# Kernel tuning notes

Measured on AMD Instinct MI355X. Metric: run time of the kernel, lower is better.

Reference implementation:

```python
import jax, jax.numpy as jnp
import numpy as np

NH, NKV, HD, RANK = 16, 4, 128, 512
DIM = NH * HD
EPS = 1.1920928955078125e-07  # torch float32 eps used by F.rms_norm default


def _rms_norm(x):
    return x * jax.lax.rsqrt(jnp.mean(x * x, axis=-1, keepdims=True) + EPS)


def _rope(x, cos, sin):
    # x: [B,H,T,HD]; cos/sin: [T,HD//2]
    h = x.shape[-1] // 2
    x1, x2 = x[..., :h], x[..., h:]
    return jnp.concatenate((x1 * cos + x2 * sin, -x1 * sin + x2 * cos), axis=-1)


def setup_inputs() -> dict:
    key = jax.random.key(0)
    ks = jax.random.split(key, 7)
    B, T = 2, 2048
    s = DIM ** -0.5
    x = jax.random.normal(ks[0], (B, T, DIM), dtype=jnp.float32)
    Wq = jax.random.normal(ks[1], (DIM, DIM), dtype=jnp.float32) * s
    Wdown = jax.random.normal(ks[2], (RANK, DIM), dtype=jnp.float32) * s
    Wkup = jax.random.normal(ks[3], (NKV * HD, RANK), dtype=jnp.float32) * s
    Wvup = jax.random.normal(ks[4], (NKV * HD, RANK), dtype=jnp.float32) * s
    Wproj = jax.random.normal(ks[5], (DIM, DIM), dtype=jnp.float32) * s
    q_gain = jnp.full((NH,), 1.0, dtype=jnp.float32)
    return {"x": x, "Wq": Wq, "Wdown": Wdown, "Wkup": Wkup, "Wvup": Wvup,
            "Wproj": Wproj, "q_gain": q_gain}


def reference(x, Wq, Wdown, Wkup, Wvup, Wproj, q_gain):
    B, T, _ = x.shape
    # q projection -> [B,NH,T,HD], rms-norm per head dim
    q = (x @ Wq.T).reshape(B, T, NH, HD).transpose(0, 2, 1, 3)
    q = _rms_norm(q)
    # low-rank latent kv
    lat = x @ Wdown.T                                   # [B,T,RANK]
    k = (lat @ Wkup.T).reshape(B, T, NKV, HD).transpose(0, 2, 1, 3)
    v = (lat @ Wvup.T).reshape(B, T, NKV, HD).transpose(0, 2, 1, 3)
    k = _rms_norm(k)
    # rotary embeddings
    inv_freq = 1.0 / (10000.0 ** (jnp.arange(0, HD, 2, dtype=jnp.float32) / HD))
    t = jnp.arange(T, dtype=jnp.float32)
    f = jnp.outer(t, inv_freq)                          # [T,HD//2]
    cos, sin = jnp.cos(f), jnp.sin(f)
    q, k = _rope(q, cos, sin), _rope(k, cos, sin)
    q = q * q_gain[None, :, None, None]
    # GQA repeat_interleave kv heads
    rep = NH // NKV
    k = jnp.repeat(k, rep, axis=1)
    v = jnp.repeat(v, rep, axis=1)
    # causal SDPA
    scores = jnp.einsum('bhqd,bhkd->bhqk', q, k) / np.sqrt(HD).astype(np.float32)
    causal = jnp.tril(jnp.ones((T, T), dtype=bool))
    scores = jnp.where(causal, scores, jnp.finfo(scores.dtype).min)
    attn = jax.nn.softmax(scores, axis=-1)
    y = jnp.einsum('bhqk,bhkd->bhqd', attn, v)          # [B,NH,T,HD]
    y = y.transpose(0, 2, 1, 3).reshape(B, T, NH * HD)
    return y @ Wproj.T
```

## Files before the change

### kernel.cpp

```cpp
#include <hip/hip_runtime.h>
#include <stdint.h>

#define B_    2
#define T_    2048
#define NH_   16
#define NKV_  4
#define HD_   128
#define RANK_ 512
#define DIM_  2048
#define BT_   (B_*T_)
#define EPS_  1.1920928955078125e-07f
#define LOG2E_ 1.4426950408889634f
#define CT_   6
#define SLOTS_PER_BH_ 204

typedef __bf16 bf16x8 __attribute__((ext_vector_type(8)));
typedef float  f32x4  __attribute__((ext_vector_type(4)));

__device__ inline unsigned short f2bf(float f) {
    unsigned int u = __float_as_uint(f);
    u += 0x7fff + ((u >> 16) & 1);
    return (unsigned short)(u >> 16);
}
__device__ inline float bf2f(unsigned short u) {
    return __uint_as_float(((unsigned int)u) << 16);
}
__device__ inline float fast_exp2(float x) { return __builtin_amdgcn_exp2f(x); }

#define GLOAD_LDS16(gp, lp)                                                        \
    __builtin_amdgcn_global_load_lds(                                              \
        (const __attribute__((address_space(1))) void*)(gp),                       \
        (__attribute__((address_space(3))) void*)(lp), 16, 0, 0)

struct CvtArgs {
    const float* src[6];
    unsigned short* dst[6];
    int start4[6];
};
__global__ __launch_bounds__(256) void cvt_all(CvtArgs a, int total4) {
    int i = blockIdx.x * 256 + threadIdx.x;
    if (i >= total4) return;
    int s = 0;
#pragma unroll
    for (int k = 1; k < 6; k++) s += (i >= a.start4[k]) ? 1 : 0;
    int j = i - a.start4[s];
    float4 v = ((const float4*)a.src[s])[j];
    ushort4 o;
    o.x = f2bf(v.x); o.y = f2bf(v.y); o.z = f2bf(v.z); o.w = f2bf(v.w);
    ((ushort4*)a.dst[s])[j] = o;
}

__device__ inline void store_out(float* p, float v) { *p = v; }
__device__ inline void store_out(unsigned short* p, float v) { *p = f2bf(v); }

template <typename OT>
__global__ __launch_bounds__(256) void gemm_bt(const unsigned short* __restrict__ A,
                                               const unsigned short* __restrict__ W,
                                               OT* __restrict__ C,
                                               int M, int N, int K) {
    __shared__ unsigned short As[2][128][32];
    __shared__ unsigned short Ws[2][128][32];
    int tid  = threadIdx.x;
    int lane = tid & 63, wave = tid >> 6;
    int quad = lane >> 4, l16 = lane & 15;
    int wm = (wave >> 1) * 64, wn = (wave & 1) * 64;
    long m0 = (long)blockIdx.y * 128, n0 = (long)blockIdx.x * 128;

    int sr = wave * 32 + (lane >> 2);
    int scl = (lane & 3) * 8;
    const unsigned short* Ag0 = A + (m0 + sr) * K + scl;
    const unsigned short* Ag1 = A + (m0 + sr + 16) * K + scl;
    const unsigned short* Wg0 = W + (n0 + sr) * K + scl;
    const unsigned short* Wg1 = W + (n0 + sr + 16) * K + scl;
    unsigned short* Al0 = &As[0][wave * 32][0];
    unsigned short* Al1 = &As[0][wave * 32 + 16][0];
    unsigned short* Wl0 = &Ws[0][wave * 32][0];
    unsigned short* Wl1 = &Ws[0][wave * 32 + 16][0];

    f32x4 acc[4][4];
#pragma unroll
    for (int i = 0; i < 4; i++)
#pragma unroll
        for (int j = 0; j < 4; j++) acc[i][j] = (f32x4){0.f, 0.f, 0.f, 0.f};

    for (int k0 = 0; k0 < K; k0 += 64) {
        __syncthreads();
        GLOAD_LDS16(Ag0 + k0, Al0);
        GLOAD_LDS16(Ag1 + k0, Al1);
        GLOAD_LDS16(Wg0 + k0, Wl0);
        GLOAD_LDS16(Wg1 + k0, Wl1);
        GLOAD_LDS16(Ag0 + k0 + 32, Al0 + 4096);
        GLOAD_LDS16(Ag1 + k0 + 32, Al1 + 4096);
        GLOAD_LDS16(Wg0 + k0 + 32, Wl0 + 4096);
        GLOAD_LDS16(Wg1 + k0 + 32, Wl1 + 4096);
        __syncthreads();
#pragma unroll
        for (int p = 0; p < 2; p++) {
            bf16x8 af[4], wf[4];
#pragma unroll
            for (int i = 0; i < 4; i++) af[i] = *(const bf16x8*)&As[p][wm + i * 16 + l16][quad * 8];
#pragma unroll
            for (int j = 0; j < 4; j++) wf[j] = *(const bf16x8*)&Ws[p][wn + j * 16 + l16][quad * 8];
#pragma unroll
            for (int i = 0; i < 4; i++)
#pragma unroll
                for (int j = 0; j < 4; j++)
                    acc[i][j] = __builtin_amdgcn_mfma_f32_16x16x32_bf16(af[i], wf[j], acc[i][j], 0, 0, 0);
        }
    }
#pragma unroll
    for (int i = 0; i < 4; i++)
#pragma unroll
        for (int j = 0; j < 4; j++)
#pragma unroll
            for (int r = 0; r < 4; r++) {
                long row = m0 + wm + i * 16 + quad * 4 + r;
                long col = n0 + wn + j * 16 + l16;
                store_out(&C[row * N + col], acc[i][j][r]);
            }
}

__global__ __launch_bounds__(256) void gemm_split(const unsigned short* __restrict__ A,
                                                  const unsigned short* __restrict__ W,
                                                  unsigned short* __restrict__ C1, int N1,
                                                  unsigned short* __restrict__ C2,
                                                  int M, int N, int K) {
    __shared__ unsigned short As[2][128][32];
    __shared__ unsigned short Ws[2][128][32];
    int tid  = threadIdx.x;
    int lane = tid & 63, wave = tid >> 6;
    int quad = lane >> 4, l16 = lane & 15;
    int wm = (wave >> 1) * 64, wn = (wave & 1) * 64;
    long m0 = (long)blockIdx.y * 128, n0 = (long)blockIdx.x * 128;

    int sr = wave * 32 + (lane >> 2);
    int scl = (lane & 3) * 8;
    const unsigned short* Ag0 = A + (m0 + sr) * K + scl;
    const unsigned short* Ag1 = A + (m0 + sr + 16) * K + scl;
    const unsigned short* Wg0 = W + (n0 + sr) * K + scl;
    const unsigned short* Wg1 = W + (n0 + sr + 16) * K + scl;
    unsigned short* Al0 = &As[0][wave * 32][0];
    unsigned short* Al1 = &As[0][wave * 32 + 16][0];
    unsigned short* Wl0 = &Ws[0][wave * 32][0];
    unsigned short* Wl1 = &Ws[0][wave * 32 + 16][0];

    f32x4 acc[4][4];
#pragma unroll
    for (int i = 0; i < 4; i++)
#pragma unroll
        for (int j = 0; j < 4; j++) acc[i][j] = (f32x4){0.f, 0.f, 0.f, 0.f};

    for (int k0 = 0; k0 < K; k0 += 64) {
        __syncthreads();
        GLOAD_LDS16(Ag0 + k0, Al0);
        GLOAD_LDS16(Ag1 + k0, Al1);
        GLOAD_LDS16(Wg0 + k0, Wl0);
        GLOAD_LDS16(Wg1 + k0, Wl1);
        GLOAD_LDS16(Ag0 + k0 + 32, Al0 + 4096);
        GLOAD_LDS16(Ag1 + k0 + 32, Al1 + 4096);
        GLOAD_LDS16(Wg0 + k0 + 32, Wl0 + 4096);
        GLOAD_LDS16(Wg1 + k0 + 32, Wl1 + 4096);
        __syncthreads();
#pragma unroll
        for (int p = 0; p < 2; p++) {
            bf16x8 af[4], wf[4];
#pragma unroll
            for (int i = 0; i < 4; i++) af[i] = *(const bf16x8*)&As[p][wm + i * 16 + l16][quad * 8];
#pragma unroll
            for (int j = 0; j < 4; j++) wf[j] = *(const bf16x8*)&Ws[p][wn + j * 16 + l16][quad * 8];
#pragma unroll
            for (int i = 0; i < 4; i++)
#pragma unroll
                for (int j = 0; j < 4; j++)
                    acc[i][j] = __builtin_amdgcn_mfma_f32_16x16x32_bf16(af[i], wf[j], acc[i][j], 0, 0, 0);
        }
    }
    unsigned short* Cb;
    long ldc, nb;
    if (n0 < N1) { Cb = C1; ldc = N1;     nb = n0; }
    else         { Cb = C2; ldc = N - N1; nb = n0 - N1; }
#pragma unroll
    for (int i = 0; i < 4; i++)
#pragma unroll
        for (int j = 0; j < 4; j++)
#pragma unroll
            for (int r = 0; r < 4; r++) {
                long row = m0 + wm + i * 16 + quad * 4 + r;
                long col = nb + wn + j * 16 + l16;
                Cb[row * ldc + col] = f2bf(acc[i][j][r]);
            }
}

__global__ __launch_bounds__(256) void prep_all(const unsigned short* __restrict__ q_lin,
                                                const unsigned short* __restrict__ kv_lin,
                                                const float* __restrict__ gain,
                                                unsigned short* __restrict__ q_bf,
                                                unsigned short* __restrict__ k_bf,
                                                unsigned short* __restrict__ vt) {
    int bid = blockIdx.x;
    if (bid < 20480) {
        bool isQ = bid < 16384;
        int nheads = isQ ? NH_ : NKV_;
        int incols = isQ ? DIM_ : 1024;
        const unsigned short* lin = isQ ? q_lin : kv_lin;
        unsigned short* out = isQ ? q_bf : k_bf;
        int base = isQ ? bid : bid - 16384;
        int r    = base * 4 + (threadIdx.x >> 6);
        int lane = threadIdx.x & 63;
        int bt = r / nheads, h = r % nheads;
        const unsigned short* ip = lin + (long)bt * incols + h * 128;
        float x1 = bf2f(ip[lane]), x2 = bf2f(ip[lane + 64]);
        float ss = x1 * x1 + x2 * x2;
#pragma unroll
        for (int off = 32; off; off >>= 1) ss += __shfl_xor(ss, off);
        float inv = rsqrtf(ss * (1.0f / 128.0f) + EPS_);
        x1 *= inv; x2 *= inv;
        int b = bt / T_, t = bt % T_;
        float freq = expf(-(float)lane * 0.14391156463f);
        float f = (float)t * freq;
        float s, c;
        sincosf(f, &s, &c);
        float g = isQ ? gain[h] * 0.08838834764831845f * LOG2E_ : 1.0f;
        float o1 = (x1 * c + x2 * s) * g;
        float o2 = (x2 * c - x1 * s) * g;
        unsigned short* op = out + ((long)(b * nheads + h) * T_ + t) * 128;
        op[lane]      = f2bf(o1);
        op[lane + 64] = f2bf(o2);
    } else {
        __shared__ unsigned short tile[32][33];
        int idx = bid - 20480;
        int tt = idx & 63, dd = (idx >> 6) & 3, bkv = idx >> 8;
        int b = bkv >> 2, kv = bkv & 3;
        int t0 = tt * 32, d0 = dd * 32;
        int tx = threadIdx.x & 31, ty = threadIdx.x >> 5;
#pragma unroll
        for (int rr = 0; rr < 32; rr += 8) {
            int t = t0 + ty + rr;
            tile[ty + rr][tx] = kv_lin[((long)(b * T_ + t)) * 1024 + 512 + kv * 128 + d0 + tx];
        }
        __syncthreads();
#pragma unroll
        for (int rr = 0; rr < 32; rr += 8) {
            int d = d0 + ty + rr;
            vt[((long)((b * NKV_ + kv) * 128 + d)) * T_ + t0 + tx] = tile[tx][ty + rr];
        }
    }
}

__global__ __launch_bounds__(256, 3) void attn_kernel(const unsigned short* __restrict__ Q,
                                                      const unsigned short* __restrict__ Km,
                                                      const unsigned short* __restrict__ Vt,
                                                      unsigned short* __restrict__ po,
                                                      float* __restrict__ pm,
                                                      float* __restrict__ pl) {
    __shared__ alignas(16) unsigned short Vs2[2][128][32];
    __shared__ alignas(16) unsigned short KsPt[4 * 32 * 72];

    int tid = threadIdx.x, lane = tid & 63, wave = tid >> 6;
    int quad = lane >> 4, l16 = lane & 15;

    int g8 = blockIdx.x & 7;
    int j5 = blockIdx.x >> 3;
    int hh = j5 / 51;
    int rem = 50 - (j5 % 51);
    int b = g8 >> 2, kvh = g8 & 3, h = kvh * 4 + hh, bh = b * 16 + h;
    int a = 0;
    while (a < 5 && 3 * (a + 1) * (a + 2) / 2 <= rem) a++;
    int off = rem - 3 * a * (a + 1) / 2;
    int nc = a + 1;
    int qb = (a == 5) ? 15 : (3 * a + off / nc);
    int c  = (a == 5) ? off : (off % nc);
    int Q0 = qb * 128 + wave * 32;

    int kt0 = c * CT_;
    int nt  = min(CT_, 2 * qb + 2 - kt0);

    const unsigned short* qp = Q + ((long)(b * NH_ + h) * T_ + Q0) * 128;
    const char* kb = (const char*)(Km + (long)(b * NKV_ + kvh) * T_ * 128);
    const char* vb = (const char*)(Vt + (long)(b * NKV_ + kvh) * 128 * (long)T_);
    char* ksB = (char*)&KsPt[0];
    char* vsB = (char*)&Vs2[0][0][0];
    unsigned short* PtW = &KsPt[wave * 2304];

    bf16x8 Qf[2][4];
#pragma unroll
    for (int u = 0; u < 2; u++)
#pragma unroll
        for (int s = 0; s < 4; s++)
            Qf[u][s] = *(const bf16x8*)&qp[(u * 16 + l16) * 128 + s * 32 + quad * 8];

    f32x4 Ot[8][2];
#pragma unroll
    for (int n = 0; n < 8; n++)
#pragma unroll
        for (int u = 0; u < 2; u++) Ot[n][u] = (f32x4){0.f, 0.f, 0.f, 0.f};
    float mr[2] = {-3.0e38f, -3.0e38f}, ls[2] = {0.f, 0.f};

    for (int kt = kt0; kt < kt0 + nt; kt++) {
        int tb = kt * 64;
        __syncthreads();
        {
            const char* kg = kb + (long)tb * 256 + wave * 64 + (lane >> 2) * 256 + (lane & 3) * 16;
            char* kl = ksB + wave * 4096 + lane * 16;
#pragma unroll
            for (int r = 0; r < 4; r++)
                GLOAD_LDS16(kg + r * 4096, kl + r * 1024);
        }
        {
            int h2 = wave >> 1;
            int D0 = (wave & 1) * 64;
#pragma unroll
            for (int r = 0; r < 4; r++) {
                int D = D0 + r * 16;
                const char* vgr = vb + (long)(D + (lane >> 2)) * 4096 + (long)tb * 2 + h2 * 64 + (lane & 3) * 16;
                char* vl = vsB + h2 * 8192 + D * 64 + lane * 16;
                GLOAD_LDS16(vgr, vl);
            }
        }
        __syncthreads();

        f32x4 sc[4][2];
#pragma unroll
        for (int j = 0; j < 4; j++)
#pragma unroll
            for (int u = 0; u < 2; u++) sc[j][u] = (f32x4){0.f, 0.f, 0.f, 0.f};
#pragma unroll
        for (int j = 0; j < 4; j++)
#pragma unroll
            for (int s = 0; s < 4; s++) {
                bf16x8 kf = *(const bf16x8*)&KsPt[s * 2048 + (j * 16 + l16) * 32 + quad * 8];
                sc[j][0] = __builtin_amdgcn_mfma_f32_16x16x32_bf16(kf, Qf[0][s], sc[j][0], 0, 0, 0);
                sc[j][1] = __builtin_amdgcn_mfma_f32_16x16x32_bf16(kf, Qf[1][s], sc[j][1], 0, 0, 0);
            }
        __syncthreads();

#pragma unroll
        for (int u = 0; u < 2; u++) {
            if (tb + 63 > Q0 + u * 16) {
                int qg = Q0 + u * 16 + l16;
#pragma unroll
                for (int j = 0; j < 4; j++)
#pragma unroll
                    for (int r = 0; r < 4; r++) {
                        int kvg = tb + j * 16 + quad * 4 + r;
                        if (kvg > qg) sc[j][u][r] = -3.0e38f;
                    }
            }
            float mx = -3.0e38f;
#pragma unroll
            for (int j = 0; j < 4; j++)
#pragma unroll
                for (int r = 0; r < 4; r++) mx = fmaxf(mx, sc[j][u][r]);
            mx = fmaxf(mx, __shfl_xor(mx, 16));
            mx = fmaxf(mx, __shfl_xor(mx, 32));
            float mnew  = fmaxf(mr[u], mx);
            float alpha = fast_exp2(mr[u] - mnew);
            float ps = 0.f;
#pragma unroll
            for (int j = 0; j < 4; j++) {
                ushort4 pk;
                float p0 = fast_exp2(sc[j][u][0] - mnew);
                float p1 = fast_exp2(sc[j][u][1] - mnew);
                float p2 = fast_exp2(sc[j][u][2] - mnew);
                float p3 = fast_exp2(sc[j][u][3] - mnew);
                ps += (p0 + p1) + (p2 + p3);
                pk.x = f2bf(p0); pk.y = f2bf(p1); pk.z = f2bf(p2); pk.w = f2bf(p3);
                *(ushort4*)&PtW[(u * 16 + l16) * 72 + j * 16 + quad * 4] = pk;
            }
            ps += __shfl_xor(ps, 16);
            ps += __shfl_xor(ps, 32);
            ls[u] = ls[u] * alpha + ps;
            mr[u] = mnew;
#pragma unroll
            for (int n = 0; n < 8; n++) Ot[n][u] *= alpha;
        }
        __threadfence_block();

#pragma unroll
        for (int h2 = 0; h2 < 2; h2++) {
            bf16x8 pf0 = *(const bf16x8*)&PtW[(0 * 16 + l16) * 72 + h2 * 32 + quad * 8];
            bf16x8 pf1 = *(const bf16x8*)&PtW[(1 * 16 + l16) * 72 + h2 * 32 + quad * 8];
#pragma unroll
            for (int n = 0; n < 8; n++) {
                bf16x8 vf = *(const bf16x8*)&Vs2[h2][n * 16 + l16][quad * 8];
                Ot[n][0] = __builtin_amdgcn_mfma_f32_16x16x32_bf16(vf, pf0, Ot[n][0], 0, 0, 0);
                Ot[n][1] = __builtin_amdgcn_mfma_f32_16x16x32_bf16(vf, pf1, Ot[n][1], 0, 0, 0);
            }
        }
    }

    long slot = (long)bh * SLOTS_PER_BH_ + 4 * (rem - c) + wave * nc + c;
#pragma unroll
    for (int half = 0; half < 2; half++) {
        __threadfence_block();
#pragma unroll
        for (int n2 = 0; n2 < 4; n2++) {
            int n = half * 4 + n2;
#pragma unroll
            for (int u = 0; u < 2; u++) {
                ushort4 pk;
                pk.x = f2bf(Ot[n][u][0]); pk.y = f2bf(Ot[n][u][1]);
                pk.z = f2bf(Ot[n][u][2]); pk.w = f2bf(Ot[n][u][3]);
                *(ushort4*)&PtW[(u * 16 + l16) * 72 + n2 * 16 + quad * 4] = pk;
            }
        }
        __threadfence_block();
#pragma unroll
        for (int rr = 0; rr < 4; rr++) {
            int qrow = rr * 8 + (lane >> 3);
            int colseg = (lane & 7) * 8;
            uint4 val = *(const uint4*)&PtW[qrow * 72 + colseg];
            *(uint4*)&po[slot * 4096 + qrow * 128 + half * 64 + colseg] = val;
        }
    }
    if (lane < 16) {
        pm[slot * 32 + lane]      = mr[0];
        pm[slot * 32 + 16 + lane] = mr[1];
        pl[slot * 32 + lane]      = ls[0];
        pl[slot * 32 + 16 + lane] = ls[1];
    }
}

__global__ __launch_bounds__(256) void attn_combine(const unsigned short* __restrict__ po,
                                                    const float* __restrict__ pm,
                                                    const float* __restrict__ pl,
                                                    unsigned short* __restrict__ Y) {
    int bh = blockIdx.x >> 6, i2 = blockIdx.x & 63;
    int qb = i2 >> 2, w = i2 & 3;
    int a = (qb == 15) ? 5 : qb / 3;
    int nc = a + 1;
    int S = 3 * a * (a + 1) / 2 + (qb - 3 * a) * nc;
    long slot0 = (long)bh * SLOTS_PER_BH_ + 4 * S + w * nc;
    int col = threadIdx.x & 127;
    int r0  = threadIdx.x >> 7;
    int b = bh >> 4, h = bh & 15;
    for (int r = r0; r < 32; r += 2) {
        float M = -3.0e38f;
        for (int c = 0; c < nc; c++) M = fmaxf(M, pm[(slot0 + c) * 32 + r]);
        float L = 0.f, acc = 0.f;
        for (int c = 0; c < nc; c++) {
            float wgt = fast_exp2(pm[(slot0 + c) * 32 + r] - M);
            L   += pl[(slot0 + c) * 32 + r] * wgt;
            acc += wgt * bf2f(po[(slot0 + c) * 4096 + r * 128 + col]);
        }
        Y[((long)b * T_ + i2 * 32 + r) * DIM_ + h * 128 + col] = f2bf(acc / L);
    }
}

extern "C" void kernel_launch(void* const* d_in, const int* in_sizes, int n_in,
                              void* d_out, int out_size, void* d_ws, size_t ws_size,
                              hipStream_t stream) {
    const float* x     = (const float*)d_in[0];
    const float* Wq    = (const float*)d_in[1];
    const float* Wdown = (const float*)d_in[2];
    const float* Wkup  = (const float*)d_in[3];
    const float* Wvup  = (const float*)d_in[4];
    const float* Wproj = (const float*)d_in[5];
    const float* qgain = (const float*)d_in[6];

    char* ws = (char*)d_ws;
    size_t off = 0;
    auto alloc = [&](size_t bytes) -> void* {
        void* p = ws + off;
        off += (bytes + 255) & ~(size_t)255;
        return p;
    };
    unsigned short* Wp_bf  = (unsigned short*)alloc((size_t)DIM_ * DIM_ * 2);
    unsigned short* q_bf   = (unsigned short*)alloc((size_t)BT_ * DIM_ * 2);
    unsigned short* k_bf   = (unsigned short*)alloc((size_t)B_ * NKV_ * T_ * 128 * 2);
    unsigned short* vT_bf  = (unsigned short*)alloc((size_t)B_ * NKV_ * T_ * 128 * 2);
    unsigned short* y_bf   = (unsigned short*)alloc((size_t)BT_ * DIM_ * 2);
    char* region2 = ws + off;
    unsigned short* x_bf   = (unsigned short*)alloc((size_t)BT_ * DIM_ * 2);
    unsigned short* Wqd_bf = (unsigned short*)alloc((size_t)2560 * DIM_ * 2);
    unsigned short* Wkv_bf = (unsigned short*)alloc((size_t)1024 * RANK_ * 2);
    unsigned short* q_lin  = (unsigned short*)alloc((size_t)BT_ * DIM_ * 2);
    unsigned short* lat_bf = (unsigned short*)alloc((size_t)BT_ * RANK_ * 2);
    unsigned short* kv_lin = (unsigned short*)alloc((size_t)BT_ * 1024 * 2);

    const size_t NSLOT = 32 * SLOTS_PER_BH_;
    unsigned short* po = (unsigned short*)region2;
    float* pm = (float*)(region2 + NSLOT * 4096 * 2);
    float* pl = pm + NSLOT * 32;

    CvtArgs ca;
    ca.src[0] = x;     ca.dst[0] = x_bf;
    ca.src[1] = Wq;    ca.dst[1] = Wqd_bf;
    ca.src[2] = Wdown; ca.dst[2] = Wqd_bf + (size_t)DIM_ * DIM_;
    ca.src[3] = Wkup;  ca.dst[3] = Wkv_bf;
    ca.src[4] = Wvup;  ca.dst[4] = Wkv_bf + (size_t)512 * RANK_;
    ca.src[5] = Wproj; ca.dst[5] = Wp_bf;
    int n4[6] = {BT_ * DIM_ / 4, DIM_ * DIM_ / 4, RANK_ * DIM_ / 4,
                 512 * RANK_ / 4, 512 * RANK_ / 4, DIM_ * DIM_ / 4};
    int acc4 = 0;
    for (int i = 0; i < 6; i++) { ca.start4[i] = acc4; acc4 += n4[i]; }
    cvt_all<<<(acc4 + 255) / 256, 256, 0, stream>>>(ca, acc4);

    gemm_split<<<dim3(2560 / 128, BT_ / 128), 256, 0, stream>>>(x_bf, Wqd_bf, q_lin, DIM_, lat_bf, BT_, 2560, DIM_);
    gemm_bt<unsigned short><<<dim3(1024 / 128, BT_ / 128), 256, 0, stream>>>(lat_bf, Wkv_bf, kv_lin, BT_, 1024, RANK_);

    prep_all<<<16384 + 4096 + 2048, 256, 0, stream>>>(q_lin, kv_lin, qgain, q_bf, k_bf, vT_bf);

    attn_kernel<<<dim3(8 * SLOTS_PER_BH_), 256, 0, stream>>>(q_bf, k_bf, vT_bf, po, pm, pl);
    attn_combine<<<dim3(32 * 64), 256, 0, stream>>>(po, pm, pl, y_bf);

    gemm_bt<float><<<dim3(DIM_ / 128, BT_ / 128), 256, 0, stream>>>(y_bf, Wp_bf, (float*)d_out, BT_, DIM_, DIM_);
}
```

Measured before the change: 398.9 us.

## Shrink attention query tile to 16 rows per wave with finer causal chunking

Each wave now handles 16 query rows instead of 32, giving a 64-row query block per workgroup. Work is re-split into twice as many causal chunks (102 per head group), and the combine kernel is updated to match. Launch bounds are raised to 4 blocks per CU and LDS shrinks. This should improve occupancy and load balance across the many CUs. The cost is that each K/V tile loaded into LDS is reused by half as many queries, which doubles global K/V traffic and the number of partial outputs.

```diff
diff --git a/kernel.cpp b/kernel.cpp
--- a/kernel.cpp
+++ b/kernel.cpp
@@ -12,7 +12,8 @@
 #define EPS_  1.1920928955078125e-07f
 #define LOG2E_ 1.4426950408889634f
 #define CT_   6
-#define SLOTS_PER_BH_ 204
+#define CHUNKS_ 102
+#define SLOTS_PER_BH_ 408
 
 typedef __bf16 bf16x8 __attribute__((ext_vector_type(8)));
 typedef float  f32x4  __attribute__((ext_vector_type(4)));
@@ -247,54 +248,48 @@
     }
 }
 
-__global__ __launch_bounds__(256, 3) void attn_kernel(const unsigned short* __restrict__ Q,
+__global__ __launch_bounds__(256, 4) void attn_kernel(const unsigned short* __restrict__ Q,
                                                       const unsigned short* __restrict__ Km,
                                                       const unsigned short* __restrict__ Vt,
                                                       unsigned short* __restrict__ po,
                                                       float* __restrict__ pm,
                                                       float* __restrict__ pl) {
     __shared__ alignas(16) unsigned short Vs2[2][128][32];
-    __shared__ alignas(16) unsigned short KsPt[4 * 32 * 72];
+    __shared__ alignas(16) unsigned short KsPt[4 * 64 * 32];
 
     int tid = threadIdx.x, lane = tid & 63, wave = tid >> 6;
     int quad = lane >> 4, l16 = lane & 15;
 
     int g8 = blockIdx.x & 7;
     int j5 = blockIdx.x >> 3;
-    int hh = j5 / 51;
-    int rem = 50 - (j5 % 51);
+    int hh = j5 / CHUNKS_;
+    int rem = (CHUNKS_ - 1) - (j5 % CHUNKS_);
     int b = g8 >> 2, kvh = g8 & 3, h = kvh * 4 + hh, bh = b * 16 + h;
-    int a = 0;
-    while (a < 5 && 3 * (a + 1) * (a + 2) / 2 <= rem) a++;
-    int off = rem - 3 * a * (a + 1) / 2;
-    int nc = a + 1;
-    int qb = (a == 5) ? 15 : (3 * a + off / nc);
-    int c  = (a == 5) ? off : (off % nc);
-    int Q0 = qb * 128 + wave * 32;
+    int qb = 0, S = 0;
+    while (S + (qb / 6 + 1) <= rem) { S += qb / 6 + 1; ++qb; }
+    int nc = qb / 6 + 1;
+    int c  = rem - S;
+    int Q0 = qb * 64 + wave * 16;
 
     int kt0 = c * CT_;
-    int nt  = min(CT_, 2 * qb + 2 - kt0);
+    int nt  = min(CT_, qb + 1 - kt0);
 
     const unsigned short* qp = Q + ((long)(b * NH_ + h) * T_ + Q0) * 128;
     const char* kb = (const char*)(Km + (long)(b * NKV_ + kvh) * T_ * 128);
     const char* vb = (const char*)(Vt + (long)(b * NKV_ + kvh) * 128 * (long)T_);
     char* ksB = (char*)&KsPt[0];
     char* vsB = (char*)&Vs2[0][0][0];
-    unsigned short* PtW = &KsPt[wave * 2304];
-
-    bf16x8 Qf[2][4];
-#pragma unroll
-    for (int u = 0; u < 2; u++)
-#pragma unroll
-        for (int s = 0; s < 4; s++)
-            Qf[u][s] = *(const bf16x8*)&qp[(u * 16 + l16) * 128 + s * 32 + quad * 8];
-
-    f32x4 Ot[8][2];
-#pragma unroll
-    for (int n = 0; n < 8; n++)
-#pragma unroll
-        for (int u = 0; u < 2; u++) Ot[n][u] = (f32x4){0.f, 0.f, 0.f, 0.f};
-    float mr[2] = {-3.0e38f, -3.0e38f}, ls[2] = {0.f, 0.f};
+    unsigned short* PtW = &KsPt[wave * 1152];
+
+    bf16x8 Qf[4];
+#pragma unroll
+    for (int s = 0; s < 4; s++)
+        Qf[s] = *(const bf16x8*)&qp[l16 * 128 + s * 32 + quad * 8];
+
+    f32x4 Ot[8];
+#pragma unroll
+    for (int n = 0; n < 8; n++) Ot[n] = (f32x4){0.f, 0.f, 0.f, 0.f};
+    float mr = -3.0e38f, ls = 0.f;
 
     for (int kt = kt0; kt < kt0 + nt; kt++) {
         int tb = kt * 64;
@@ -319,105 +314,92 @@
         }
         __syncthreads();
 
-        f32x4 sc[4][2];
-#pragma unroll
-        for (int j = 0; j < 4; j++)
-#pragma unroll
-            for (int u = 0; u < 2; u++) sc[j][u] = (f32x4){0.f, 0.f, 0.f, 0.f};
+        f32x4 sc[4];
+#pragma unroll
+        for (int j = 0; j < 4; j++) sc[j] = (f32x4){0.f, 0.f, 0.f, 0.f};
 #pragma unroll
         for (int j = 0; j < 4; j++)
 #pragma unroll
             for (int s = 0; s < 4; s++) {
                 bf16x8 kf = *(const bf16x8*)&KsPt[s * 2048 + (j * 16 + l16) * 32 + quad * 8];
-                sc[j][0] = __builtin_amdgcn_mfma_f32_16x16x32_bf16(kf, Qf[0][s], sc[j][0], 0, 0, 0);
-                sc[j][1] = __builtin_amdgcn_mfma_f32_16x16x32_bf16(kf, Qf[1][s], sc[j][1], 0, 0, 0);
+                sc[j] = __builtin_amdgcn_mfma_f32_16x16x32_bf16(kf, Qf[s], sc[j], 0, 0, 0);
             }
         __syncthreads();
 
-#pragma unroll
-        for (int u = 0; u < 2; u++) {
-            if (tb + 63 > Q0 + u * 16) {
-                int qg = Q0 + u * 16 + l16;
-#pragma unroll
-                for (int j = 0; j < 4; j++)
-#pragma unroll
-                    for (int r = 0; r < 4; r++) {
-                        int kvg = tb + j * 16 + quad * 4 + r;
-                        if (kvg > qg) sc[j][u][r] = -3.0e38f;
-                    }
-            }
-            float mx = -3.0e38f;
+        if (tb + 63 > Q0) {
+            int qg = Q0 + l16;
 #pragma unroll
             for (int j = 0; j < 4; j++)
 #pragma unroll
-                for (int r = 0; r < 4; r++) mx = fmaxf(mx, sc[j][u][r]);
-            mx = fmaxf(mx, __shfl_xor(mx, 16));
-            mx = fmaxf(mx, __shfl_xor(mx, 32));
-            float mnew  = fmaxf(mr[u], mx);
-            float alpha = fast_exp2(mr[u] - mnew);
-            float ps = 0.f;
-#pragma unroll
-            for (int j = 0; j < 4; j++) {
-                ushort4 pk;
-                float p0 = fast_exp2(sc[j][u][0] - mnew);
-                float p1 = fast_exp2(sc[j][u][1] - mnew);
-                float p2 = fast_exp2(sc[j][u][2] - mnew);
-                float p3 = fast_exp2(sc[j][u][3] - mnew);
-                ps += (p0 + p1) + (p2 + p3);
-                pk.x = f2bf(p0); pk.y = f2bf(p1); pk.z = f2bf(p2); pk.w = f2bf(p3);
-                *(ushort4*)&PtW[(u * 16 + l16) * 72 + j * 16 + quad * 4] = pk;
-            }
-            ps += __shfl_xor(ps, 16);
-            ps += __shfl_xor(ps, 32);
-            ls[u] = ls[u] * alpha + ps;
-            mr[u] = mnew;
-#pragma unroll
-            for (int n = 0; n < 8; n++) Ot[n][u] *= alpha;
-        }
+                for (int r = 0; r < 4; r++) {
+                    int kvg = tb + j * 16 + quad * 4 + r;
+                    if (kvg > qg) sc[j][r] = -3.0e38f;
+                }
+        }
+        float mx = -3.0e38f;
+#pragma unroll
+        for (int j = 0; j < 4; j++)
+#pragma unroll
+            for (int r = 0; r < 4; r++) mx = fmaxf(mx, sc[j][r]);
+        mx = fmaxf(mx, __shfl_xor(mx, 16));
+        mx = fmaxf(mx, __shfl_xor(mx, 32));
+        float mnew  = fmaxf(mr, mx);
+        float alpha = fast_exp2(mr - mnew);
+        float ps = 0.f;
+#pragma unroll
+        for (int j = 0; j < 4; j++) {
+            ushort4 pk;
+            float p0 = fast_exp2(sc[j][0] - mnew);
+            float p1 = fast_exp2(sc[j][1] - mnew);
+            float p2 = fast_exp2(sc[j][2] - mnew);
+            float p3 = fast_exp2(sc[j][3] - mnew);
+            ps += (p0 + p1) + (p2 + p3);
+            pk.x = f2bf(p0); pk.y = f2bf(p1); pk.z = f2bf(p2); pk.w = f2bf(p3);
+            *(ushort4*)&PtW[l16 * 72 + j * 16 + quad * 4] = pk;
+        }
+        ps += __shfl_xor(ps, 16);
+        ps += __shfl_xor(ps, 32);
+        ls = ls * alpha + ps;
+        mr = mnew;
+#pragma unroll
+        for (int n = 0; n < 8; n++) Ot[n] *= alpha;
         __threadfence_block();
 
 #pragma unroll
         for (int h2 = 0; h2 < 2; h2++) {
-            bf16x8 pf0 = *(const bf16x8*)&PtW[(0 * 16 + l16) * 72 + h2 * 32 + quad * 8];
-            bf16x8 pf1 = *(const bf16x8*)&PtW[(1 * 16 + l16) * 72 + h2 * 32 + quad * 8];
+            bf16x8 pf = *(const bf16x8*)&PtW[l16 * 72 + h2 * 32 + quad * 8];
 #pragma unroll
             for (int n = 0; n < 8; n++) {
                 bf16x8 vf = *(const bf16x8*)&Vs2[h2][n * 16 + l16][quad * 8];
-                Ot[n][0] = __builtin_amdgcn_mfma_f32_16x16x32_bf16(vf, pf0, Ot[n][0], 0, 0, 0);
-                Ot[n][1] = __builtin_amdgcn_mfma_f32_16x16x32_bf16(vf, pf1, Ot[n][1], 0, 0, 0);
+                Ot[n] = __builtin_amdgcn_mfma_f32_16x16x32_bf16(vf, pf, Ot[n], 0, 0, 0);
             }
         }
     }
 
-    long slot = (long)bh * SLOTS_PER_BH_ + 4 * (rem - c) + wave * nc + c;
+    long slot = (long)bh * SLOTS_PER_BH_ + 4 * S + wave * nc + c;
 #pragma unroll
     for (int half = 0; half < 2; half++) {
         __threadfence_block();
 #pragma unroll
         for (int n2 = 0; n2 < 4; n2++) {
             int n = half * 4 + n2;
-#pragma unroll
-            for (int u = 0; u < 2; u++) {
-                ushort4 pk;
-                pk.x = f2bf(Ot[n][u][0]); pk.y = f2bf(Ot[n][u][1]);
-                pk.z = f2bf(Ot[n][u][2]); pk.w = f2bf(Ot[n][u][3]);
-                *(ushort4*)&PtW[(u * 16 + l16) * 72 + n2 * 16 + quad * 4] = pk;
-            }
+            ushort4 pk;
+            pk.x = f2bf(Ot[n][0]); pk.y = f2bf(Ot[n][1]);
+            pk.z = f2bf(Ot[n][2]); pk.w = f2bf(Ot[n][3]);
+            *(ushort4*)&PtW[l16 * 72 + n2 * 16 + quad * 4] = pk;
         }
         __threadfence_block();
 #pragma unroll
-        for (int rr = 0; rr < 4; rr++) {
+        for (int rr = 0; rr < 2; rr++) {
             int qrow = rr * 8 + (lane >> 3);
             int colseg = (lane & 7) * 8;
             uint4 val = *(const uint4*)&PtW[qrow * 72 + colseg];
-            *(uint4*)&po[slot * 4096 + qrow * 128 + half * 64 + colseg] = val;
+            *(uint4*)&po[slot * 2048 + qrow * 128 + half * 64 + colseg] = val;
         }
     }
     if (lane < 16) {
-        pm[slot * 32 + lane]      = mr[0];
-        pm[slot * 32 + 16 + lane] = mr[1];
-        pl[slot * 32 + lane]      = ls[0];
-        pl[slot * 32 + 16 + lane] = ls[1];
+        pm[slot * 16 + lane] = mr;
+        pl[slot * 16 + lane] = ls;
     }
 }
 
@@ -425,25 +407,25 @@
                                                     const float* __restrict__ pm,
                                                     const float* __restrict__ pl,
                                                     unsigned short* __restrict__ Y) {
-    int bh = blockIdx.x >> 6, i2 = blockIdx.x & 63;
+    int bh = blockIdx.x >> 7, i2 = blockIdx.x & 127;
     int qb = i2 >> 2, w = i2 & 3;
-    int a = (qb == 15) ? 5 : qb / 3;
+    int a = qb / 6, bb = qb % 6;
+    int S = qb + 3 * a * (a - 1) + a * bb;
     int nc = a + 1;
-    int S = 3 * a * (a + 1) / 2 + (qb - 3 * a) * nc;
     long slot0 = (long)bh * SLOTS_PER_BH_ + 4 * S + w * nc;
     int col = threadIdx.x & 127;
     int r0  = threadIdx.x >> 7;
     int b = bh >> 4, h = bh & 15;
-    for (int r = r0; r < 32; r += 2) {
+    for (int r = r0; r < 16; r += 2) {
         float M = -3.0e38f;
-        for (int c = 0; c < nc; c++) M = fmaxf(M, pm[(slot0 + c) * 32 + r]);
+        for (int c = 0; c < nc; c++) M = fmaxf(M, pm[(slot0 + c) * 16 + r]);
         float L = 0.f, acc = 0.f;
         for (int c = 0; c < nc; c++) {
-            float wgt = fast_exp2(pm[(slot0 + c) * 32 + r] - M);
-            L   += pl[(slot0 + c) * 32 + r] * wgt;
-            acc += wgt * bf2f(po[(slot0 + c) * 4096 + r * 128 + col]);
-        }
-        Y[((long)b * T_ + i2 * 32 + r) * DIM_ + h * 128 + col] = f2bf(acc / L);
+            float wgt = fast_exp2(pm[(slot0 + c) * 16 + r] - M);
+            L   += pl[(slot0 + c) * 16 + r] * wgt;
+            acc += wgt * bf2f(po[(slot0 + c) * 2048 + r * 128 + col]);
+        }
+        Y[((long)b * T_ + i2 * 16 + r) * DIM_ + h * 128 + col] = f2bf(acc / L);
     }
 }
 
@@ -480,8 +462,8 @@
 
     const size_t NSLOT = 32 * SLOTS_PER_BH_;
     unsigned short* po = (unsigned short*)region2;
-    float* pm = (float*)(region2 + NSLOT * 4096 * 2);
-    float* pl = pm + NSLOT * 32;
+    float* pm = (float*)(region2 + NSLOT * 2048 * 2);
+    float* pl = pm + NSLOT * 16;
 
     CvtArgs ca;
     ca.src[0] = x;     ca.dst[0] = x_bf;
@@ -502,7 +484,7 @@
     prep_all<<<16384 + 4096 + 2048, 256, 0, stream>>>(q_lin, kv_lin, qgain, q_bf, k_bf, vT_bf);
 
     attn_kernel<<<dim3(8 * SLOTS_PER_BH_), 256, 0, stream>>>(q_bf, k_bf, vT_bf, po, pm, pl);
-    attn_combine<<<dim3(32 * 64), 256, 0, stream>>>(po, pm, pl, y_bf);
+    attn_combine<<<dim3(32 * 128), 256, 0, stream>>>(po, pm, pl, y_bf);
 
     gemm_bt<float><<<dim3(DIM_ / 128, BT_ / 128), 256, 0, stream>>>(y_bf, Wp_bf, (float*)d_out, BT_, DIM_, DIM_);
 }
```

After: 374.3 us. 1.07x faster.

## XOR-swizzle LDS tiles in GEMMs and attention, reload Q per tile, raise occupancy

Applied to the files above, without the earlier changes.

Applies an XOR swizzle to the 16-byte column chunks written into LDS by global_load_lds and read back by the MFMA fragment loads, in both GEMM kernels and in the attention K/V tiles, to cut LDS bank conflicts. The attention kernel no longer holds Q fragments in registers for the whole loop. It reloads them from global/cache each KV tile and raises launch bounds to 4 blocks per CU, trading extra Q loads for lower register pressure and higher occupancy.

```diff
diff --git a/kernel.cpp b/kernel.cpp
--- a/kernel.cpp
+++ b/kernel.cpp
@@ -32,6 +32,7 @@
         (const __attribute__((address_space(1))) void*)(gp),                       \
         (__attribute__((address_space(3))) void*)(lp), 16, 0, 0)
 
+
 struct CvtArgs {
     const float* src[6];
     unsigned short* dst[6];
@@ -63,11 +64,12 @@
     int tid  = threadIdx.x;
     int lane = tid & 63, wave = tid >> 6;
     int quad = lane >> 4, l16 = lane & 15;
+    int sw   = (l16 >> 1) & 3;
     int wm = (wave >> 1) * 64, wn = (wave & 1) * 64;
     long m0 = (long)blockIdx.y * 128, n0 = (long)blockIdx.x * 128;
 
-    int sr = wave * 32 + (lane >> 2);
-    int scl = (lane & 3) * 8;
+    int sr  = wave * 32 + (lane >> 2);
+    int scl = (((lane & 3) ^ ((lane >> 3) & 3))) * 8;
     const unsigned short* Ag0 = A + (m0 + sr) * K + scl;
     const unsigned short* Ag1 = A + (m0 + sr + 16) * K + scl;
     const unsigned short* Wg0 = W + (n0 + sr) * K + scl;
@@ -98,9 +100,9 @@
         for (int p = 0; p < 2; p++) {
             bf16x8 af[4], wf[4];
 #pragma unroll
-            for (int i = 0; i < 4; i++) af[i] = *(const bf16x8*)&As[p][wm + i * 16 + l16][quad * 8];
-#pragma unroll
-            for (int j = 0; j < 4; j++) wf[j] = *(const bf16x8*)&Ws[p][wn + j * 16 + l16][quad * 8];
+            for (int i = 0; i < 4; i++) af[i] = *(const bf16x8*)&As[p][wm + i * 16 + l16][(quad ^ sw) * 8];
+#pragma unroll
+            for (int j = 0; j < 4; j++) wf[j] = *(const bf16x8*)&Ws[p][wn + j * 16 + l16][(quad ^ sw) * 8];
 #pragma unroll
             for (int i = 0; i < 4; i++)
 #pragma unroll
@@ -130,11 +132,12 @@
     int tid  = threadIdx.x;
     int lane = tid & 63, wave = tid >> 6;
     int quad = lane >> 4, l16 = lane & 15;
+    int sw   = (l16 >> 1) & 3;
     int wm = (wave >> 1) * 64, wn = (wave & 1) * 64;
     long m0 = (long)blockIdx.y * 128, n0 = (long)blockIdx.x * 128;
 
-    int sr = wave * 32 + (lane >> 2);
-    int scl = (lane & 3) * 8;
+    int sr  = wave * 32 + (lane >> 2);
+    int scl = (((lane & 3) ^ ((lane >> 3) & 3))) * 8;
     const unsigned short* Ag0 = A + (m0 + sr) * K + scl;
     const unsigned short* Ag1 = A + (m0 + sr + 16) * K + scl;
     const unsigned short* Wg0 = W + (n0 + sr) * K + scl;
@@ -165,9 +168,9 @@
         for (int p = 0; p < 2; p++) {
             bf16x8 af[4], wf[4];
 #pragma unroll
-            for (int i = 0; i < 4; i++) af[i] = *(const bf16x8*)&As[p][wm + i * 16 + l16][quad * 8];
-#pragma unroll
-            for (int j = 0; j < 4; j++) wf[j] = *(const bf16x8*)&Ws[p][wn + j * 16 + l16][quad * 8];
+            for (int i = 0; i < 4; i++) af[i] = *(const bf16x8*)&As[p][wm + i * 16 + l16][(quad ^ sw) * 8];
+#pragma unroll
+            for (int j = 0; j < 4; j++) wf[j] = *(const bf16x8*)&Ws[p][wn + j * 16 + l16][(quad ^ sw) * 8];
 #pragma unroll
             for (int i = 0; i < 4; i++)
 #pragma unroll
@@ -247,7 +250,7 @@
     }
 }
 
-__global__ __launch_bounds__(256, 3) void attn_kernel(const unsigned short* __restrict__ Q,
+__global__ __launch_bounds__(256, 4) void attn_kernel(const unsigned short* __restrict__ Q,
                                                       const unsigned short* __restrict__ Km,
                                                       const unsigned short* __restrict__ Vt,
                                                       unsigned short* __restrict__ po,
@@ -258,6 +261,8 @@
 
     int tid = threadIdx.x, lane = tid & 63, wave = tid >> 6;
     int quad = lane >> 4, l16 = lane & 15;
+    int sw   = (l16 >> 1) & 3;
+    int csw  = ((lane & 3) ^ ((lane >> 3) & 3));
 
     int g8 = blockIdx.x & 7;
     int j5 = blockIdx.x >> 3;
@@ -282,13 +287,6 @@
     char* vsB = (char*)&Vs2[0][0][0];
     unsigned short* PtW = &KsPt[wave * 2304];
 
-    bf16x8 Qf[2][4];
-#pragma unroll
-    for (int u = 0; u < 2; u++)
-#pragma unroll
-        for (int s = 0; s < 4; s++)
-            Qf[u][s] = *(const bf16x8*)&qp[(u * 16 + l16) * 128 + s * 32 + quad * 8];
-
     f32x4 Ot[8][2];
 #pragma unroll
     for (int n = 0; n < 8; n++)
@@ -300,7 +298,7 @@
         int tb = kt * 64;
         __syncthreads();
         {
-            const char* kg = kb + (long)tb * 256 + wave * 64 + (lane >> 2) * 256 + (lane & 3) * 16;
+            const char* kg = kb + (long)tb * 256 + wave * 64 + (lane >> 2) * 256 + csw * 16;
             char* kl = ksB + wave * 4096 + lane * 16;
 #pragma unroll
             for (int r = 0; r < 4; r++)
@@ -312,7 +310,7 @@
 #pragma unroll
             for (int r = 0; r < 4; r++) {
                 int D = D0 + r * 16;
-                const char* vgr = vb + (long)(D + (lane >> 2)) * 4096 + (long)tb * 2 + h2 * 64 + (lane & 3) * 16;
+                const char* vgr = vb + (long)(D + (lane >> 2)) * 4096 + (long)tb * 2 + h2 * 64 + csw * 16;
                 char* vl = vsB + h2 * 8192 + D * 64 + lane * 16;
                 GLOAD_LDS16(vgr, vl);
             }
@@ -325,13 +323,16 @@
 #pragma unroll
             for (int u = 0; u < 2; u++) sc[j][u] = (f32x4){0.f, 0.f, 0.f, 0.f};
 #pragma unroll
-        for (int j = 0; j < 4; j++)
-#pragma unroll
-            for (int s = 0; s < 4; s++) {
-                bf16x8 kf = *(const bf16x8*)&KsPt[s * 2048 + (j * 16 + l16) * 32 + quad * 8];
-                sc[j][0] = __builtin_amdgcn_mfma_f32_16x16x32_bf16(kf, Qf[0][s], sc[j][0], 0, 0, 0);
-                sc[j][1] = __builtin_amdgcn_mfma_f32_16x16x32_bf16(kf, Qf[1][s], sc[j][1], 0, 0, 0);
-            }
+        for (int s = 0; s < 4; s++) {
+            bf16x8 q0 = *(const bf16x8*)&qp[l16 * 128 + s * 32 + quad * 8];
+            bf16x8 q1 = *(const bf16x8*)&qp[(16 + l16) * 128 + s * 32 + quad * 8];
+#pragma unroll
+            for (int j = 0; j < 4; j++) {
+                bf16x8 kf = *(const bf16x8*)&KsPt[s * 2048 + (j * 16 + l16) * 32 + (quad ^ sw) * 8];
+                sc[j][0] = __builtin_amdgcn_mfma_f32_16x16x32_bf16(kf, q0, sc[j][0], 0, 0, 0);
+                sc[j][1] = __builtin_amdgcn_mfma_f32_16x16x32_bf16(kf, q1, sc[j][1], 0, 0, 0);
+            }
+        }
         __syncthreads();
 
 #pragma unroll
@@ -382,7 +383,7 @@
             bf16x8 pf1 = *(const bf16x8*)&PtW[(1 * 16 + l16) * 72 + h2 * 32 + quad * 8];
 #pragma unroll
             for (int n = 0; n < 8; n++) {
-                bf16x8 vf = *(const bf16x8*)&Vs2[h2][n * 16 + l16][quad * 8];
+                bf16x8 vf = *(const bf16x8*)&Vs2[h2][n * 16 + l16][(quad ^ sw) * 8];
                 Ot[n][0] = __builtin_amdgcn_mfma_f32_16x16x32_bf16(vf, pf0, Ot[n][0], 0, 0, 0);
                 Ot[n][1] = __builtin_amdgcn_mfma_f32_16x16x32_bf16(vf, pf1, Ot[n][1], 0, 0, 0);
             }
```

New measurement: 458.1 us. 14.8% more time.
